# Kernel optimization log

Hardware: AMD Instinct MI355X
Metric: run time of the kernel (lower is better)

The kernel has to match this reference:

```python
import jax, jax.numpy as jnp
import numpy as np


def setup_inputs() -> dict:
    key = jax.random.key(0)
    k1, k2, k3 = jax.random.split(key, 3)
    B, N, D, F = 4, 4096, 128, 128
    features = jax.random.normal(k1, (B, N, D), dtype=jnp.float32)
    A = jax.random.uniform(k2, (B, N, N), dtype=jnp.float32)
    weight = jax.random.normal(k3, (D, F), dtype=jnp.float32) * (6.0 / (D + F)) ** 0.5
    bias = jnp.zeros((F,), dtype=jnp.float32)
    return {"features": features, "A": A, "weight": weight, "bias": bias}


def reference(features, A, weight, bias):
    # aggregate: per-batch adjacency matmul  [B,N,N] @ [B,N,D] -> [B,N,D]
    agg = jnp.einsum("bnm,bmd->bnd", A, features)
    # linear transform + bias + relu  [B,N,D] @ [D,F] -> [B,N,F]
    out = jnp.einsum("bnd,df->bnf", agg, weight) + bias
    return jax.nn.relu(out)
```

## Files before the change

kernel.cpp:

```cpp
#include <hip/hip_runtime.h>

typedef __attribute__((ext_vector_type(4))) float  float4v;
typedef __attribute__((ext_vector_type(4))) short  short4v;
typedef __attribute__((ext_vector_type(8))) short  short8v;
typedef __attribute__((ext_vector_type(4))) float  f32x4;

__device__ __forceinline__ short f2bf(float f) {
  unsigned int u = __float_as_uint(f);
  u = u + 0x7fffu + ((u >> 16) & 1u);
  return (short)(u >> 16);
}

__device__ __forceinline__ int swz(int row, int k, int ld) {
  return row * ld + (k ^ ((row & 7) << 3));
}

__device__ __forceinline__ void gll16(const void* g, void* l) {
  __builtin_amdgcn_global_load_lds(
      (const __attribute__((address_space(1))) unsigned int*)g,
      (__attribute__((address_space(3))) unsigned int*)l, 16, 0, 0);
}

__device__ __forceinline__ short8v cvt8(float4v v0, float4v v1) {
  short8v s;
  s[0]=f2bf(v0[0]); s[1]=f2bf(v0[1]); s[2]=f2bf(v0[2]); s[3]=f2bf(v0[3]);
  s[4]=f2bf(v1[0]); s[5]=f2bf(v1[1]); s[6]=f2bf(v1[2]); s[7]=f2bf(v1[3]);
  return s;
}

__global__ __launch_bounds__(256) void k1_feat_x_w(
    const float* __restrict__ feat, const float* __restrict__ W,
    short* __restrict__ ht, int N) {
  __shared__ short Fs[64 * 128];
  __shared__ short Ws[128 * 128];
  const int t = threadIdx.x;
  const int batch = blockIdx.y;
  const int m0 = blockIdx.x * 64;
  const float* fb = feat + (size_t)batch * N * 128;

  {
    const int row = t >> 4;
    const int d = (t & 15) * 8;
#pragma unroll
    for (int i = 0; i < 4; ++i) {
      const int r = i * 16 + row;
      const float4v* src = (const float4v*)(fb + (size_t)(m0 + r) * 128 + d);
      *(short8v*)(&Fs[swz(r, d, 128)]) = cvt8(src[0], src[1]);
    }
  }
  {
    const int f = t >> 1;
    const int dbase = (t & 1) * 64;
#pragma unroll
    for (int g = 0; g < 16; ++g) {
      const int d = dbase + g * 4;
      short4v s;
#pragma unroll
      for (int i = 0; i < 4; ++i) s[i] = f2bf(W[(size_t)(d + i) * 128 + f]);
      *(short4v*)(&Ws[swz(f, d, 128)]) = s;
    }
  }
  __syncthreads();

  const int lane = t & 63, wid = t >> 6;
  const int wm = (wid >> 1) * 32, wn = (wid & 1) * 64;
  const int lr = lane & 15, lk = (lane >> 4) * 8;

  f32x4 acc[2][4];
#pragma unroll
  for (int i = 0; i < 2; ++i)
#pragma unroll
    for (int j = 0; j < 4; ++j) acc[i][j] = (f32x4){0.f, 0.f, 0.f, 0.f};

#pragma unroll
  for (int kk = 0; kk < 4; ++kk) {
    const int k = kk * 32 + lk;
    short8v a[2], b[4];
#pragma unroll
    for (int mi = 0; mi < 2; ++mi)
      a[mi] = *(const short8v*)(&Fs[swz(wm + mi * 16 + lr, k, 128)]);
#pragma unroll
    for (int ni = 0; ni < 4; ++ni)
      b[ni] = *(const short8v*)(&Ws[swz(wn + ni * 16 + lr, k, 128)]);
#pragma unroll
    for (int mi = 0; mi < 2; ++mi)
#pragma unroll
      for (int ni = 0; ni < 4; ++ni)
        acc[mi][ni] = __builtin_amdgcn_mfma_f32_16x16x32_bf16(a[mi], b[ni], acc[mi][ni], 0, 0, 0);
  }

  short* hb = ht + (size_t)batch * 128 * N;
#pragma unroll
  for (int mi = 0; mi < 2; ++mi) {
    const int m = m0 + wm + mi * 16 + (lane >> 4) * 4;
#pragma unroll
    for (int ni = 0; ni < 4; ++ni) {
      const int f = wn + ni * 16 + lr;
      short4v s;
#pragma unroll
      for (int r = 0; r < 4; ++r) s[r] = f2bf(acc[mi][ni][r]);
      *(short4v*)(hb + (size_t)f * N + m) = s;
    }
  }
}

__global__ __launch_bounds__(256) void k2_a_x_h(
    const float* __restrict__ A, const short* __restrict__ ht,
    const float* __restrict__ bias, float* __restrict__ out, int N) {
  __shared__ short As[2][32 * 64];
  __shared__ short Hs[2][128 * 64];
  const int t = threadIdx.x;
  const int batch = blockIdx.y;
  const int m0 = blockIdx.x * 32;
  const float* Ab = A + (size_t)batch * N * N;
  const short* hb = ht + (size_t)batch * 128 * N;

  const int lane = t & 63, wid = t >> 6;
  const int wm = (wid >> 1) * 16, wn = (wid & 1) * 64;
  const int lr = lane & 15, lk = (lane >> 4) * 8;

  const int arow = t >> 3;
  const int akc = (t & 7) * 8;

  const int hf = lane >> 3;
  const int hks = (lane & 7) * 8;

  float4v va0, va1;

  auto loadA = [&](int k0) {
    const float* p = Ab + (size_t)(m0 + arow) * N + k0 + akc;
    va0 = ((const float4v*)p)[0];
    va1 = ((const float4v*)p)[1];
  };
  auto writeA = [&](int buf) {
    *(short8v*)(&As[buf][swz(arow, akc, 64)]) = cvt8(va0, va1);
  };
  auto stageH = [&](int k0, int buf) {
#pragma unroll
    for (int i = 0; i < 4; ++i) {
      const int fb8 = (wid * 4 + i) * 8;
      const int f = fb8 + hf;
      const short* g = hb + (size_t)f * N + k0 + (hks ^ (hf << 3));
      gll16(g, &Hs[buf][fb8 * 64]);
    }
  };

  f32x4 acc[4];
#pragma unroll
  for (int j = 0; j < 4; ++j) acc[j] = (f32x4){0.f, 0.f, 0.f, 0.f};

  loadA(0);
  stageH(0, 0);
  writeA(0);
  __syncthreads();

  const int NT = N / 64;
  for (int tt = 0; tt < NT; ++tt) {
    const int cur = tt & 1;
    const bool pf = (tt + 1 < NT);
    if (pf) {
      loadA((tt + 1) * 64);
      stageH((tt + 1) * 64, cur ^ 1);
    }
#pragma unroll
    for (int kk = 0; kk < 2; ++kk) {
      const int k = kk * 32 + lk;
      short8v a = *(const short8v*)(&As[cur][swz(wm + lr, k, 64)]);
      short8v b[4];
#pragma unroll
      for (int ni = 0; ni < 4; ++ni)
        b[ni] = *(const short8v*)(&Hs[cur][swz(wn + ni * 16 + lr, k, 64)]);
#pragma unroll
      for (int ni = 0; ni < 4; ++ni)
        acc[ni] = __builtin_amdgcn_mfma_f32_16x16x32_bf16(a, b[ni], acc[ni], 0, 0, 0);
    }
    if (pf) writeA(cur ^ 1);
    __syncthreads();
  }

  float* ob = out + (size_t)batch * N * 128;
#pragma unroll
  for (int ni = 0; ni < 4; ++ni) {
    const int f = wn + ni * 16 + lr;
    const float bv = bias[f];
    const int mbase = m0 + wm + (lane >> 4) * 4;
#pragma unroll
    for (int r = 0; r < 4; ++r)
      ob[(size_t)(mbase + r) * 128 + f] = fmaxf(acc[ni][r] + bv, 0.f);
  }
}

extern "C" void kernel_launch(void* const* d_in, const int* in_sizes, int n_in,
                              void* d_out, int out_size, void* d_ws, size_t ws_size,
                              hipStream_t stream) {
  const float* feat = (const float*)d_in[0];
  const float* A    = (const float*)d_in[1];
  const float* W    = (const float*)d_in[2];
  const float* bias = (const float*)d_in[3];
  float* out = (float*)d_out;

  const int featN = in_sizes[0];
  const int aN    = in_sizes[1];
  const int BN    = featN / 128;
  const int N     = aN / BN;
  const int Bb    = BN / N;

  short* ht = (short*)d_ws;

  dim3 g1(N / 64, Bb), g2(N / 32, Bb), blk(256);
  hipLaunchKernelGGL(k1_feat_x_w, g1, blk, 0, stream, feat, W, ht, N);
  hipLaunchKernelGGL(k2_a_x_h, g2, blk, 0, stream, A, ht, bias, out, N);
}
```

Measured before the change: 85.72 us.

## Rewrite GCN kernels with register-direct loads, split-K waves and XCD-aware tile mapping

Main GEMM kernel drops LDS staging. A tiles are loaded straight into registers with a register double buffer, and H^T fragments are read directly from global memory. Waves split K in half and reduce through LDS. Each block now computes a 64-row tile with launch_bounds(256,1), and block IDs are remapped across 8 XCDs. Weight transpose and conversion moves into a separate small kernel, the feature GEMM loads A fragments directly from global, and the rounding uses the HIP bf16 intrinsic. The aim is to cut LDS traffic and barriers in the bandwidth-bound A read, at the risk of less coalesced H loads and lower occupancy.

```diff
diff --git a/kernel.cpp b/kernel.cpp
--- a/kernel.cpp
+++ b/kernel.cpp
@@ -1,4 +1,5 @@
 #include <hip/hip_runtime.h>
+#include <hip/hip_bf16.h>
 
 typedef __attribute__((ext_vector_type(4))) float  float4v;
 typedef __attribute__((ext_vector_type(4))) short  short4v;
@@ -6,19 +7,8 @@
 typedef __attribute__((ext_vector_type(4))) float  f32x4;
 
 __device__ __forceinline__ short f2bf(float f) {
-  unsigned int u = __float_as_uint(f);
-  u = u + 0x7fffu + ((u >> 16) & 1u);
-  return (short)(u >> 16);
-}
-
-__device__ __forceinline__ int swz(int row, int k, int ld) {
-  return row * ld + (k ^ ((row & 7) << 3));
-}
-
-__device__ __forceinline__ void gll16(const void* g, void* l) {
-  __builtin_amdgcn_global_load_lds(
-      (const __attribute__((address_space(1))) unsigned int*)g,
-      (__attribute__((address_space(3))) unsigned int*)l, 16, 0, 0);
+  __hip_bfloat16 h = __float2bfloat16(f);
+  return *reinterpret_cast<short*>(&h);
 }
 
 __device__ __forceinline__ short8v cvt8(float4v v0, float4v v1) {
@@ -28,165 +18,167 @@
   return s;
 }
 
+__device__ __forceinline__ int swz(int row, int k, int ld) {
+  return row * ld + (k ^ ((row & 7) << 3));
+}
+
+__global__ __launch_bounds__(256) void k0_wt(const float* __restrict__ W,
+                                             short* __restrict__ wt) {
+  const int task = blockIdx.x * 256 + threadIdx.x;
+  const int f = task & 127;
+  const int dc = (task >> 7) * 8;
+  short8v s;
+#pragma unroll
+  for (int j = 0; j < 8; ++j) s[j] = f2bf(W[(size_t)(dc + j) * 128 + f]);
+  *(short8v*)(wt + (size_t)f * 128 + dc) = s;
+}
+
 __global__ __launch_bounds__(256) void k1_feat_x_w(
-    const float* __restrict__ feat, const float* __restrict__ W,
+    const float* __restrict__ feat, const short* __restrict__ wt,
     short* __restrict__ ht, int N) {
-  __shared__ short Fs[64 * 128];
   __shared__ short Ws[128 * 128];
   const int t = threadIdx.x;
   const int batch = blockIdx.y;
   const int m0 = blockIdx.x * 64;
   const float* fb = feat + (size_t)batch * N * 128;
 
-  {
-    const int row = t >> 4;
-    const int d = (t & 15) * 8;
-#pragma unroll
-    for (int i = 0; i < 4; ++i) {
-      const int r = i * 16 + row;
-      const float4v* src = (const float4v*)(fb + (size_t)(m0 + r) * 128 + d);
-      *(short8v*)(&Fs[swz(r, d, 128)]) = cvt8(src[0], src[1]);
+#pragma unroll
+  for (int it = 0; it < 8; ++it) {
+    const int idx = it * 256 + t;
+    const int f = idx >> 4;
+    const int dc = (idx & 15) * 8;
+    short8v v = *(const short8v*)(wt + (size_t)f * 128 + dc);
+    *(short8v*)(&Ws[swz(f, dc, 128)]) = v;
+  }
+  __syncthreads();
+
+  const int lane = t & 63, wid = t >> 6;
+  const int lr = lane & 15, lk = (lane >> 4) * 8;
+  const float* pa = fb + (size_t)(m0 + wid * 16 + lr) * 128 + lk;
+
+  f32x4 acc[8];
+#pragma unroll
+  for (int j = 0; j < 8; ++j) acc[j] = (f32x4){0.f, 0.f, 0.f, 0.f};
+
+#pragma unroll
+  for (int kk = 0; kk < 4; ++kk) {
+    float4v v0 = ((const float4v*)(pa + kk * 32))[0];
+    float4v v1 = ((const float4v*)(pa + kk * 32))[1];
+    short8v a = cvt8(v0, v1);
+#pragma unroll
+    for (int ni = 0; ni < 8; ++ni) {
+      short8v b = *(const short8v*)(&Ws[swz(ni * 16 + lr, kk * 32 + lk, 128)]);
+      acc[ni] = __builtin_amdgcn_mfma_f32_16x16x32_bf16(a, b, acc[ni], 0, 0, 0);
     }
   }
-  {
-    const int f = t >> 1;
-    const int dbase = (t & 1) * 64;
-#pragma unroll
-    for (int g = 0; g < 16; ++g) {
-      const int d = dbase + g * 4;
-      short4v s;
-#pragma unroll
-      for (int i = 0; i < 4; ++i) s[i] = f2bf(W[(size_t)(d + i) * 128 + f]);
-      *(short4v*)(&Ws[swz(f, d, 128)]) = s;
-    }
-  }
-  __syncthreads();
-
-  const int lane = t & 63, wid = t >> 6;
-  const int wm = (wid >> 1) * 32, wn = (wid & 1) * 64;
-  const int lr = lane & 15, lk = (lane >> 4) * 8;
-
-  f32x4 acc[2][4];
-#pragma unroll
-  for (int i = 0; i < 2; ++i)
-#pragma unroll
-    for (int j = 0; j < 4; ++j) acc[i][j] = (f32x4){0.f, 0.f, 0.f, 0.f};
-
-#pragma unroll
-  for (int kk = 0; kk < 4; ++kk) {
-    const int k = kk * 32 + lk;
-    short8v a[2], b[4];
-#pragma unroll
-    for (int mi = 0; mi < 2; ++mi)
-      a[mi] = *(const short8v*)(&Fs[swz(wm + mi * 16 + lr, k, 128)]);
-#pragma unroll
-    for (int ni = 0; ni < 4; ++ni)
-      b[ni] = *(const short8v*)(&Ws[swz(wn + ni * 16 + lr, k, 128)]);
-#pragma unroll
-    for (int mi = 0; mi < 2; ++mi)
-#pragma unroll
-      for (int ni = 0; ni < 4; ++ni)
-        acc[mi][ni] = __builtin_amdgcn_mfma_f32_16x16x32_bf16(a[mi], b[ni], acc[mi][ni], 0, 0, 0);
-  }
 
   short* hb = ht + (size_t)batch * 128 * N;
-#pragma unroll
-  for (int mi = 0; mi < 2; ++mi) {
-    const int m = m0 + wm + mi * 16 + (lane >> 4) * 4;
-#pragma unroll
-    for (int ni = 0; ni < 4; ++ni) {
-      const int f = wn + ni * 16 + lr;
-      short4v s;
-#pragma unroll
-      for (int r = 0; r < 4; ++r) s[r] = f2bf(acc[mi][ni][r]);
-      *(short4v*)(hb + (size_t)f * N + m) = s;
-    }
-  }
-}
-
-__global__ __launch_bounds__(256) void k2_a_x_h(
+  const int m = m0 + wid * 16 + (lane >> 4) * 4;
+#pragma unroll
+  for (int ni = 0; ni < 8; ++ni) {
+    const int f = ni * 16 + lr;
+    short4v s;
+#pragma unroll
+    for (int r = 0; r < 4; ++r) s[r] = f2bf(acc[ni][r]);
+    *(short4v*)(hb + (size_t)f * N + m) = s;
+  }
+}
+
+__global__ __launch_bounds__(256, 1) void k2_a_x_h(
     const float* __restrict__ A, const short* __restrict__ ht,
     const float* __restrict__ bias, float* __restrict__ out, int N) {
-  __shared__ short As[2][32 * 64];
-  __shared__ short Hs[2][128 * 64];
+  __shared__ f32x4 Cred[2][16 * 64];
   const int t = threadIdx.x;
-  const int batch = blockIdx.y;
-  const int m0 = blockIdx.x * 32;
+
+  const int nwg = gridDim.x * gridDim.y;
+  int wg = blockIdx.x + gridDim.x * blockIdx.y;
+  if ((nwg & 7) == 0) wg = (wg & 7) * (nwg >> 3) + (wg >> 3);
+  const int mtiles = gridDim.x;
+  const int batch = wg / mtiles;
+  const int m0 = (wg - batch * mtiles) * 64;
+
   const float* Ab = A + (size_t)batch * N * N;
   const short* hb = ht + (size_t)batch * 128 * N;
 
   const int lane = t & 63, wid = t >> 6;
-  const int wm = (wid >> 1) * 16, wn = (wid & 1) * 64;
+  const int mp = wid & 1;
+  const int kh = wid >> 1;
   const int lr = lane & 15, lk = (lane >> 4) * 8;
-
-  const int arow = t >> 3;
-  const int akc = (t & 7) * 8;
-
-  const int hf = lane >> 3;
-  const int hks = (lane & 7) * 8;
-
-  float4v va0, va1;
-
-  auto loadA = [&](int k0) {
-    const float* p = Ab + (size_t)(m0 + arow) * N + k0 + akc;
-    va0 = ((const float4v*)p)[0];
-    va1 = ((const float4v*)p)[1];
+  const int khalf = N >> 1;
+
+  const float* pa0 = Ab + (size_t)(m0 + mp * 32 + lr) * N + kh * khalf + lk;
+  const float* pa1 = pa0 + (size_t)16 * N;
+  const short* pb  = hb + (size_t)lr * N + kh * khalf + lk;
+
+  f32x4 acc[2][8];
+#pragma unroll
+  for (int i = 0; i < 2; ++i)
+#pragma unroll
+    for (int j = 0; j < 8; ++j) acc[i][j] = (f32x4){0.f, 0.f, 0.f, 0.f};
+
+  const int NSTEP = khalf >> 6;
+
+  float4v buf0[8], buf1[8];
+
+  auto loadA = [&](float4v (&buf)[8], int k0) {
+    const float* p0 = pa0 + k0;
+    const float* p1 = pa1 + k0;
+    buf[0] = ((const float4v*)p0)[0];        buf[1] = ((const float4v*)p0)[1];
+    buf[2] = ((const float4v*)(p0 + 32))[0]; buf[3] = ((const float4v*)(p0 + 32))[1];
+    buf[4] = ((const float4v*)p1)[0];        buf[5] = ((const float4v*)p1)[1];
+    buf[6] = ((const float4v*)(p1 + 32))[0]; buf[7] = ((const float4v*)(p1 + 32))[1];
   };
-  auto writeA = [&](int buf) {
-    *(short8v*)(&As[buf][swz(arow, akc, 64)]) = cvt8(va0, va1);
-  };
-  auto stageH = [&](int k0, int buf) {
-#pragma unroll
-    for (int i = 0; i < 4; ++i) {
-      const int fb8 = (wid * 4 + i) * 8;
-      const int f = fb8 + hf;
-      const short* g = hb + (size_t)f * N + k0 + (hks ^ (hf << 3));
-      gll16(g, &Hs[buf][fb8 * 64]);
+  auto step = [&](float4v (&buf)[8], int k0) {
+    short8v a[2][2];
+    a[0][0] = cvt8(buf[0], buf[1]);
+    a[0][1] = cvt8(buf[2], buf[3]);
+    a[1][0] = cvt8(buf[4], buf[5]);
+    a[1][1] = cvt8(buf[6], buf[7]);
+#pragma unroll
+    for (int kk = 0; kk < 2; ++kk) {
+      short8v b[8];
+#pragma unroll
+      for (int ni = 0; ni < 8; ++ni)
+        b[ni] = *(const short8v*)(pb + (size_t)ni * 16 * N + k0 + kk * 32);
+#pragma unroll
+      for (int ni = 0; ni < 8; ++ni) {
+        acc[0][ni] = __builtin_amdgcn_mfma_f32_16x16x32_bf16(a[0][kk], b[ni], acc[0][ni], 0, 0, 0);
+        acc[1][ni] = __builtin_amdgcn_mfma_f32_16x16x32_bf16(a[1][kk], b[ni], acc[1][ni], 0, 0, 0);
+      }
     }
   };
 
-  f32x4 acc[4];
-#pragma unroll
-  for (int j = 0; j < 4; ++j) acc[j] = (f32x4){0.f, 0.f, 0.f, 0.f};
-
-  loadA(0);
-  stageH(0, 0);
-  writeA(0);
+  loadA(buf0, 0);
+  for (int s = 0; s < NSTEP; s += 2) {
+    if (s + 1 < NSTEP) loadA(buf1, (s + 1) * 64);
+    step(buf0, s * 64);
+    if (s + 2 < NSTEP) loadA(buf0, (s + 2) * 64);
+    if (s + 1 < NSTEP) step(buf1, (s + 1) * 64);
+  }
+
+  if (kh == 1) {
+#pragma unroll
+    for (int ms = 0; ms < 2; ++ms)
+#pragma unroll
+      for (int ni = 0; ni < 8; ++ni)
+        Cred[mp][(ms * 8 + ni) * 64 + lane] = acc[ms][ni];
+  }
   __syncthreads();
-
-  const int NT = N / 64;
-  for (int tt = 0; tt < NT; ++tt) {
-    const int cur = tt & 1;
-    const bool pf = (tt + 1 < NT);
-    if (pf) {
-      loadA((tt + 1) * 64);
-      stageH((tt + 1) * 64, cur ^ 1);
+  if (kh == 0) {
+    float* ob = out + (size_t)batch * N * 128;
+#pragma unroll
+    for (int ms = 0; ms < 2; ++ms) {
+      const int mbase = m0 + mp * 32 + ms * 16 + (lane >> 4) * 4;
+#pragma unroll
+      for (int ni = 0; ni < 8; ++ni) {
+        const f32x4 o = Cred[mp][(ms * 8 + ni) * 64 + lane];
+        const int f = ni * 16 + lr;
+        const float bv = bias[f];
+#pragma unroll
+        for (int r = 0; r < 4; ++r)
+          ob[(size_t)(mbase + r) * 128 + f] = fmaxf(acc[ms][ni][r] + o[r] + bv, 0.f);
+      }
     }
-#pragma unroll
-    for (int kk = 0; kk < 2; ++kk) {
-      const int k = kk * 32 + lk;
-      short8v a = *(const short8v*)(&As[cur][swz(wm + lr, k, 64)]);
-      short8v b[4];
-#pragma unroll
-      for (int ni = 0; ni < 4; ++ni)
-        b[ni] = *(const short8v*)(&Hs[cur][swz(wn + ni * 16 + lr, k, 64)]);
-#pragma unroll
-      for (int ni = 0; ni < 4; ++ni)
-        acc[ni] = __builtin_amdgcn_mfma_f32_16x16x32_bf16(a, b[ni], acc[ni], 0, 0, 0);
-    }
-    if (pf) writeA(cur ^ 1);
-    __syncthreads();
-  }
-
-  float* ob = out + (size_t)batch * N * 128;
-#pragma unroll
-  for (int ni = 0; ni < 4; ++ni) {
-    const int f = wn + ni * 16 + lr;
-    const float bv = bias[f];
-    const int mbase = m0 + wm + (lane >> 4) * 4;
-#pragma unroll
-    for (int r = 0; r < 4; ++r)
-      ob[(size_t)(mbase + r) * 128 + f] = fmaxf(acc[ni][r] + bv, 0.f);
   }
 }
 
@@ -205,9 +197,11 @@
   const int N     = aN / BN;
   const int Bb    = BN / N;
 
-  short* ht = (short*)d_ws;
-
-  dim3 g1(N / 64, Bb), g2(N / 32, Bb), blk(256);
-  hipLaunchKernelGGL(k1_feat_x_w, g1, blk, 0, stream, feat, W, ht, N);
-  hipLaunchKernelGGL(k2_a_x_h, g2, blk, 0, stream, A, ht, bias, out, N);
-}
+  short* wt = (short*)d_ws;
+  short* ht = wt + 128 * 128;
+
+  dim3 blk(256);
+  hipLaunchKernelGGL(k0_wt, dim3(8), blk, 0, stream, W, wt);
+  hipLaunchKernelGGL(k1_feat_x_w, dim3(N / 64, Bb), blk, 0, stream, feat, wt, ht, N);
+  hipLaunchKernelGGL(k2_a_x_h, dim3(N / 64, Bb), blk, 0, stream, A, ht, bias, out, N);
+}
```

Result: slower. 120.9 us (+41.0%).
